# Kernel optimization log

Hardware: AMD Instinct MI355X
Metric: run time of the kernel (lower is better)

Reference implementation:

```python
import jax, jax.numpy as jnp
import numpy as np
from jax import lax

SOBEL = jnp.array([[-1., -1., -1.], [-1., 8., -1.], [-1., -1., -1.]], dtype=jnp.float32)


def setup_inputs() -> dict:
    key = jax.random.key(0)
    ks = jax.random.split(key, 7)
    B, C, H, W = 8, 256, 224, 224
    return {
        "x": jax.random.normal(ks[0], (B, C, H, W), dtype=jnp.float32),
        "spatial_w": jax.random.normal(ks[1], (1, C), dtype=jnp.float32) * 0.05,
        "spatial_b": jax.random.normal(ks[2], (1,), dtype=jnp.float32) * 0.05,
        "cc1_w": jax.random.normal(ks[3], (C // 4, C), dtype=jnp.float32) * 0.05,
        "cc1_b": jax.random.normal(ks[4], (C // 4,), dtype=jnp.float32) * 0.05,
        "cc2_w": jax.random.normal(ks[5], (C, C // 4), dtype=jnp.float32) * 0.05,
        "cc2_b": jax.random.normal(ks[6], (C,), dtype=jnp.float32) * 0.05,
    }


def reference(x, spatial_w, spatial_b, cc1_w, cc1_b, cc2_w, cc2_b):
    B, C, H, W = x.shape
    # spatial attention: 1x1 conv C->1, sigmoid -> [B,1,H,W]
    spatial = jax.nn.sigmoid(
        jnp.einsum('bchw,oc->bohw', x, spatial_w) + spatial_b[None, :, None, None]
    )
    # channel attention: global avg pool + SE bottleneck, sigmoid -> [B,C,1,1]
    avg = jnp.mean(x, axis=(2, 3))                       # [B,C]
    h = jax.nn.relu(avg @ cc1_w.T + cc1_b)               # [B,C//4]
    channel = jax.nn.sigmoid(h @ cc2_w.T + cc2_b)        # [B,C]
    channel = channel[:, :, None, None]
    # edge attention: depthwise 3x3 Sobel (fixed kernel, no grad), sigmoid
    sobel_k = jnp.broadcast_to(SOBEL[None, None], (C, 1, 3, 3))
    edge_raw = lax.conv_general_dilated(
        x, sobel_k, window_strides=(1, 1), padding=((1, 1), (1, 1)),
        dimension_numbers=('NCHW', 'OIHW', 'NCHW'), feature_group_count=C)
    edge = jax.nn.sigmoid(lax.stop_gradient(edge_raw))
    return x * (spatial * channel * edge)
```

## Files before the change

### kernel.cpp

```cpp
#include <hip/hip_runtime.h>
#include <math.h>

#define BB 8
#define CC 256
#define HH 224
#define WW 224
#define HWSZ (HH * WW)
#define HW2  (HWSZ / 2)
#define C4 64

__device__ __forceinline__ float sigmoidf_(float z) {
    return 1.0f / (1.0f + __expf(-z));
}

__global__ __launch_bounds__(256) void k1_spatial_avg(
    const float* __restrict__ x, const float* __restrict__ sw,
    const float* __restrict__ sb, float* __restrict__ spatial_sig,
    float* __restrict__ avgsum)
{
    __shared__ float tile[4][32][65];
    __shared__ float chansum[CC];
    const int tid  = threadIdx.x;
    const int wave = tid >> 6;
    const int lane = tid & 63;
    const int b    = blockIdx.y;
    const int p2   = blockIdx.x * 256 + tid;
    const float2* xp = (const float2*)(x + (size_t)b * CC * HWSZ) + p2;

    chansum[tid] = 0.f;
    __syncthreads();

    float s0 = 0.f, s1 = 0.f;
    #pragma unroll 1
    for (int ct = 0; ct < 8; ++ct) {
        #pragma unroll
        for (int jj = 0; jj < 4; ++jj) {
            float2 v[8];
            #pragma unroll
            for (int u = 0; u < 8; ++u)
                v[u] = xp[(size_t)(ct * 32 + jj * 8 + u) * HW2];
            #pragma unroll
            for (int u = 0; u < 8; ++u) {
                const int c = ct * 32 + jj * 8 + u;
                const float w = sw[c];
                s0 = fmaf(v[u].x, w, s0);
                s1 = fmaf(v[u].y, w, s1);
                tile[wave][jj * 8 + u][lane] = v[u].x + v[u].y;
            }
        }
        __syncthreads();
        const int cl  = lane & 31;
        const int seg = lane >> 5;
        float part = 0.f;
        #pragma unroll 8
        for (int j = 0; j < 32; ++j)
            part += tile[wave][cl][seg * 32 + j];
        part += __shfl_xor(part, 32, 64);
        if (lane < 32) atomicAdd(&chansum[ct * 32 + cl], part);
        __syncthreads();
    }

    const float bias = sb[0];
    float2 o;
    o.x = sigmoidf_(s0 + bias);
    o.y = sigmoidf_(s1 + bias);
    ((float2*)(spatial_sig + (size_t)b * HWSZ))[p2] = o;

    __syncthreads();
    atomicAdd(&avgsum[b * CC + tid], chansum[tid]);
}

__global__ __launch_bounds__(64) void k2_channel(
    const float* __restrict__ avgsum, const float* __restrict__ w1,
    const float* __restrict__ b1, const float* __restrict__ w2,
    const float* __restrict__ b2, float* __restrict__ channel_sig)
{
    __shared__ float avg[CC];
    __shared__ float hsh[C4];
    const int b = blockIdx.x;
    const int t = threadIdx.x;
    const float inv = 1.0f / (float)HWSZ;
    for (int c = t; c < CC; c += 64) avg[c] = avgsum[b * CC + c] * inv;
    __syncthreads();

    float acc = b1[t];
    const float* wrow = w1 + t * CC;
    #pragma unroll 4
    for (int c = 0; c < CC; ++c) acc = fmaf(avg[c], wrow[c], acc);
    hsh[t] = fmaxf(acc, 0.f);
    __syncthreads();

    for (int c = t; c < CC; c += 64) {
        float a = b2[c];
        const float* w2r = w2 + c * C4;
        #pragma unroll
        for (int o = 0; o < C4; ++o) a = fmaf(hsh[o], w2r[o], a);
        channel_sig[b * CC + c] = sigmoidf_(a);
    }
}

__device__ __forceinline__ float4 horiz4(float4 v, int q) {
    float l  = __shfl(v.w, q - 1, 64);
    float rr = __shfl(v.x, q + 1, 64);
    l  = (q == 0)  ? 0.f : l;
    rr = (q == 55) ? 0.f : rr;
    float4 h;
    h.x = l   + v.x + v.y;
    h.y = v.x + v.y + v.z;
    h.z = v.y + v.z + v.w;
    h.w = v.z + v.w + rr;
    return h;
}

__global__ __launch_bounds__(256) void k3_out(
    const float* __restrict__ x, const float* __restrict__ spatial_sig,
    const float* __restrict__ channel_sig, float* __restrict__ out)
{
    const int bc = blockIdx.y;
    const int b  = bc >> 8;
    const int strip = blockIdx.x * 4 + threadIdx.y;
    const int q  = threadIdx.x;
    if (q >= 56) return;
    const int r0   = strip * 28;
    const int col0 = q * 4;

    const float* plane    = x           + (size_t)bc * HWSZ;
    const float* sp_plane = spatial_sig + (size_t)b  * HWSZ;
    float*       o_plane  = out         + (size_t)bc * HWSZ;
    const float  ch = channel_sig[bc];

    const float4 z4 = make_float4(0.f, 0.f, 0.f, 0.f);
    float4 vm = (r0 > 0) ? *(const float4*)(plane + (r0 - 1) * WW + col0) : z4;
    float4 vc = *(const float4*)(plane + (r0    ) * WW + col0);
    float4 vp = *(const float4*)(plane + (r0 + 1) * WW + col0);
    float4 vn = *(const float4*)(plane + (r0 + 2) * WW + col0);
    float4 sp = *(const float4*)(sp_plane + r0 * WW + col0);

    float4 hs_m = horiz4(vm, q);
    float4 hs_c = horiz4(vc, q);

    #pragma unroll 4
    for (int r = r0; r < r0 + 28; ++r) {
        float4 vq = (r + 3 < HH)
                  ? *(const float4*)(plane + (r + 3) * WW + col0) : z4;
        float4 sp_n = (r + 1 < HH)
                  ? *(const float4*)(sp_plane + (r + 1) * WW + col0) : z4;
        float4 hs_p = horiz4(vp, q);

        float4 o;
        o.x = vc.x * sp.x * ch * sigmoidf_(9.f * vc.x - (hs_m.x + hs_c.x + hs_p.x));
        o.y = vc.y * sp.y * ch * sigmoidf_(9.f * vc.y - (hs_m.y + hs_c.y + hs_p.y));
        o.z = vc.z * sp.z * ch * sigmoidf_(9.f * vc.z - (hs_m.z + hs_c.z + hs_p.z));
        o.w = vc.w * sp.w * ch * sigmoidf_(9.f * vc.w - (hs_m.w + hs_c.w + hs_p.w));
        *(float4*)(o_plane + r * WW + col0) = o;

        vc = vp; vp = vn; vn = vq;
        hs_m = hs_c; hs_c = hs_p;
        sp = sp_n;
    }
}

extern "C" void kernel_launch(void* const* d_in, const int* in_sizes, int n_in,
                              void* d_out, int out_size, void* d_ws, size_t ws_size,
                              hipStream_t stream) {
    const float* x  = (const float*)d_in[0];
    const float* sw = (const float*)d_in[1];
    const float* sb = (const float*)d_in[2];
    const float* w1 = (const float*)d_in[3];
    const float* b1 = (const float*)d_in[4];
    const float* w2 = (const float*)d_in[5];
    const float* b2 = (const float*)d_in[6];
    float* out = (float*)d_out;

    float* spatial_sig = (float*)d_ws;
    float* avgsum      = spatial_sig + (size_t)BB * HWSZ;
    float* channel_sig = avgsum + BB * CC;

    hipMemsetAsync(avgsum, 0, BB * CC * sizeof(float), stream);

    k1_spatial_avg<<<dim3(HWSZ / 512, BB), 256, 0, stream>>>(
        x, sw, sb, spatial_sig, avgsum);
    k2_channel<<<dim3(BB), 64, 0, stream>>>(
        avgsum, w1, b1, w2, b2, channel_sig);
    k3_out<<<dim3(2, BB * CC), dim3(64, 4), 0, stream>>>(
        x, spatial_sig, channel_sig, out);
}
```

Before: 804.5 us.

## Software-pipeline k1 channel loads, drop block barriers, use nontemporal loads/stores in k3

k1 now double-buffers its per-group loads of 8 channels, prefetching the next group while the current one is accumulated. It also removes the two __syncthreads per 32-channel tile, relying on each wave only reading its own shared-memory tile slice. k3 switches the x loads and output stores to nontemporal builtins so this streaming data does not displace spatial_sig and other reused lines in the caches. The risks are extra register pressure from the prefetch buffers and the need for intra-wave LDS ordering to hold without explicit barriers.

```diff
diff --git a/kernel.cpp b/kernel.cpp
--- a/kernel.cpp
+++ b/kernel.cpp
@@ -8,6 +8,8 @@
 #define HWSZ (HH * WW)
 #define HW2  (HWSZ / 2)
 #define C4 64
+
+typedef float f4 __attribute__((ext_vector_type(4)));
 
 __device__ __forceinline__ float sigmoidf_(float z) {
     return 1.0f / (1.0f + __expf(-z));
@@ -23,6 +25,8 @@
     const int tid  = threadIdx.x;
     const int wave = tid >> 6;
     const int lane = tid & 63;
+    const int cl   = lane & 31;
+    const int seg  = lane >> 5;
     const int b    = blockIdx.y;
     const int p2   = blockIdx.x * 256 + tid;
     const float2* xp = (const float2*)(x + (size_t)b * CC * HWSZ) + p2;
@@ -30,34 +34,36 @@
     chansum[tid] = 0.f;
     __syncthreads();
 
+    float2 v[8], vn[8];
+    #pragma unroll
+    for (int u = 0; u < 8; ++u) v[u] = xp[(size_t)u * HW2];
+
     float s0 = 0.f, s1 = 0.f;
-    #pragma unroll 1
-    for (int ct = 0; ct < 8; ++ct) {
-        #pragma unroll
-        for (int jj = 0; jj < 4; ++jj) {
-            float2 v[8];
+    #pragma unroll 4
+    for (int g = 0; g < 32; ++g) {
+        if (g < 31) {
             #pragma unroll
             for (int u = 0; u < 8; ++u)
-                v[u] = xp[(size_t)(ct * 32 + jj * 8 + u) * HW2];
+                vn[u] = xp[(size_t)((g + 1) * 8 + u) * HW2];
+        }
+        #pragma unroll
+        for (int u = 0; u < 8; ++u) {
+            const float w = sw[g * 8 + u];
+            s0 = fmaf(v[u].x, w, s0);
+            s1 = fmaf(v[u].y, w, s1);
+            tile[wave][(g & 3) * 8 + u][lane] = v[u].x + v[u].y;
+        }
+        if ((g & 3) == 3) {
+            float part = 0.f;
             #pragma unroll
-            for (int u = 0; u < 8; ++u) {
-                const int c = ct * 32 + jj * 8 + u;
-                const float w = sw[c];
-                s0 = fmaf(v[u].x, w, s0);
-                s1 = fmaf(v[u].y, w, s1);
-                tile[wave][jj * 8 + u][lane] = v[u].x + v[u].y;
-            }
+            for (int j = 0; j < 32; ++j)
+                part += tile[wave][cl][seg * 32 + j];
+            part += __shfl_xor(part, 32, 64);
+            if (lane < 32)
+                atomicAdd(&chansum[(g >> 2) * 32 + cl], part);
         }
-        __syncthreads();
-        const int cl  = lane & 31;
-        const int seg = lane >> 5;
-        float part = 0.f;
-        #pragma unroll 8
-        for (int j = 0; j < 32; ++j)
-            part += tile[wave][cl][seg * 32 + j];
-        part += __shfl_xor(part, 32, 64);
-        if (lane < 32) atomicAdd(&chansum[ct * 32 + cl], part);
-        __syncthreads();
+        #pragma unroll
+        for (int u = 0; u < 8; ++u) v[u] = vn[u];
     }
 
     const float bias = sb[0];
@@ -99,12 +105,16 @@
     }
 }
 
-__device__ __forceinline__ float4 horiz4(float4 v, int q) {
+__device__ __forceinline__ f4 ldnt(const float* p) {
+    return __builtin_nontemporal_load((const f4*)p);
+}
+
+__device__ __forceinline__ f4 horiz4(f4 v, int q) {
     float l  = __shfl(v.w, q - 1, 64);
     float rr = __shfl(v.x, q + 1, 64);
     l  = (q == 0)  ? 0.f : l;
     rr = (q == 55) ? 0.f : rr;
-    float4 h;
+    f4 h;
     h.x = l   + v.x + v.y;
     h.y = v.x + v.y + v.z;
     h.z = v.y + v.z + v.w;
@@ -129,30 +139,28 @@
     float*       o_plane  = out         + (size_t)bc * HWSZ;
     const float  ch = channel_sig[bc];
 
-    const float4 z4 = make_float4(0.f, 0.f, 0.f, 0.f);
-    float4 vm = (r0 > 0) ? *(const float4*)(plane + (r0 - 1) * WW + col0) : z4;
-    float4 vc = *(const float4*)(plane + (r0    ) * WW + col0);
-    float4 vp = *(const float4*)(plane + (r0 + 1) * WW + col0);
-    float4 vn = *(const float4*)(plane + (r0 + 2) * WW + col0);
-    float4 sp = *(const float4*)(sp_plane + r0 * WW + col0);
+    const f4 z4 = {0.f, 0.f, 0.f, 0.f};
+    f4 vm = (r0 > 0) ? ldnt(plane + (r0 - 1) * WW + col0) : z4;
+    f4 vc = ldnt(plane + (r0    ) * WW + col0);
+    f4 vp = ldnt(plane + (r0 + 1) * WW + col0);
+    f4 vn = ldnt(plane + (r0 + 2) * WW + col0);
+    f4 sp = *(const f4*)(sp_plane + r0 * WW + col0);
 
-    float4 hs_m = horiz4(vm, q);
-    float4 hs_c = horiz4(vc, q);
+    f4 hs_m = horiz4(vm, q);
+    f4 hs_c = horiz4(vc, q);
 
     #pragma unroll 4
     for (int r = r0; r < r0 + 28; ++r) {
-        float4 vq = (r + 3 < HH)
-                  ? *(const float4*)(plane + (r + 3) * WW + col0) : z4;
-        float4 sp_n = (r + 1 < HH)
-                  ? *(const float4*)(sp_plane + (r + 1) * WW + col0) : z4;
-        float4 hs_p = horiz4(vp, q);
+        f4 vq = (r + 3 < HH) ? ldnt(plane + (r + 3) * WW + col0) : z4;
+        f4 sp_n = (r + 1 < HH) ? *(const f4*)(sp_plane + (r + 1) * WW + col0) : z4;
+        f4 hs_p = horiz4(vp, q);
 
-        float4 o;
+        f4 o;
         o.x = vc.x * sp.x * ch * sigmoidf_(9.f * vc.x - (hs_m.x + hs_c.x + hs_p.x));
         o.y = vc.y * sp.y * ch * sigmoidf_(9.f * vc.y - (hs_m.y + hs_c.y + hs_p.y));
         o.z = vc.z * sp.z * ch * sigmoidf_(9.f * vc.z - (hs_m.z + hs_c.z + hs_p.z));
         o.w = vc.w * sp.w * ch * sigmoidf_(9.f * vc.w - (hs_m.w + hs_c.w + hs_p.w));
-        *(float4*)(o_plane + r * WW + col0) = o;
+        __builtin_nontemporal_store(o, (f4*)(o_plane + r * WW + col0));
 
         vc = vp; vp = vn; vn = vq;
         hs_m = hs_c; hs_c = hs_p;
```

After: 787.5 us. 1.02x faster.
